# Kernel tuning notes

Hardware: AMD Instinct MI355X
Metric: run time of the kernel (lower is better)

The kernel has to match this reference:

```python
import jax, jax.numpy as jnp
import numpy as np
import math

B, S, K, D, H, LH, W, L = 8, 2048, 128, 512, 8, 4, 128, 4
DH = D // H           # 64, head dim
NW = S // W           # 16 windows
NUM_STEPS = 1000
RESCALE = 4000.0


def setup_inputs() -> dict:
    key = jax.random.key(0)
    ks = iter(jax.random.split(key, 48))
    def rn(shape, s=0.02):
        return jax.random.normal(next(ks), shape, dtype=jnp.float32) * s
    return {
        "x": jax.random.normal(next(ks), (B, S, K), dtype=jnp.float32),
        "t": jax.random.randint(next(ks), (B,), 0, NUM_STEPS, dtype=jnp.int32),
        "token_w": rn((K, D)), "token_b": jnp.zeros((D,), jnp.float32),
        "ax1": rn((NW, D), 1.0), "ax2": rn((W, D), 1.0),
        "time_w1": rn((D, 4 * D)), "time_b1": jnp.zeros((4 * D,), jnp.float32),
        "time_w2": rn((4 * D, D)), "time_b2": jnp.zeros((D,), jnp.float32),
        "ln1_g": jnp.ones((L, D), jnp.float32), "ln1_b": jnp.zeros((L, D), jnp.float32),
        "wq": rn((L, D, D)), "wk": rn((L, D, D)), "wv": rn((L, D, D)),
        "wo": rn((L, D, D)), "wo_b": jnp.zeros((L, D), jnp.float32),
        "ln2_g": jnp.ones((L, D), jnp.float32), "ln2_b": jnp.zeros((L, D), jnp.float32),
        "ff_w1": rn((L, D, 4 * D)), "ff_b1": jnp.zeros((L, 4 * D), jnp.float32),
        "ff_w2": rn((L, 4 * D, D)), "ff_b2": jnp.zeros((L, D), jnp.float32),
        "norm_g": jnp.ones((D,), jnp.float32), "norm_b": jnp.zeros((D,), jnp.float32),
        "out_w": rn((D, K)), "out_b": jnp.zeros((K,), jnp.float32),
        "alpha": jax.random.normal(next(ks), (1,), dtype=jnp.float32),
    }


def _layernorm(x, g, b, eps=1e-5):
    mu = x.mean(-1, keepdims=True)
    var = ((x - mu) ** 2).mean(-1, keepdims=True)
    return (x - mu) * jax.lax.rsqrt(var + eps) * g + b


def _mish(x):
    return x * jnp.tanh(jax.nn.softplus(x))


def _sinusoidal(t):
    # SinusoidalPosEmb(dim=D, num_steps=NUM_STEPS, rescale_steps=4000)
    tt = t.astype(jnp.float32) / NUM_STEPS * RESCALE
    half = D // 2
    freqs = jnp.exp(jnp.arange(half, dtype=jnp.float32) * (-math.log(10000.0) / (half - 1)))
    e = tt[:, None] * freqs[None, :]
    return jnp.concatenate([jnp.sin(e), jnp.cos(e)], axis=-1)  # (B, D)


def _linear_attn(q, k, v):
    # non-causal kernelized linear attention; q,k,v: (B, h, S, dh)
    scale = DH ** -0.25
    q = jax.nn.softmax(q * scale, axis=-1)   # softmax over feature dim
    k = jax.nn.softmax(k * scale, axis=-2)   # softmax over sequence dim
    ctx = jnp.einsum('bhnd,bhne->bhde', k, v)
    return jnp.einsum('bhnd,bhde->bhne', q, ctx)


def _local_attn(q, k, v):
    # windowed softmax attention, window W, look_backward=1, look_forward=1
    b, h = q.shape[0], q.shape[1]
    qw = q.reshape(b, h, NW, W, DH) * (DH ** -0.5)
    def look_around(x):
        xw = x.reshape(b, h, NW, W, DH)
        xp = jnp.pad(xw, ((0, 0), (0, 0), (1, 1), (0, 0), (0, 0)))
        # keys of windows [i-1, i, i+1] -> (b, h, NW, 3W, dh)
        return jnp.concatenate([xp[:, :, :-2], xp[:, :, 1:-1], xp[:, :, 2:]], axis=3)
    kw, vw = look_around(k), look_around(v)
    win = jnp.arange(NW)[:, None] + (jnp.arange(3 * W) // W)[None, :] - 1  # (NW, 3W)
    valid = (win >= 0) & (win < NW)
    dots = jnp.einsum('bhnwd,bhnkd->bhnwk', qw, kw)
    mask_value = -jnp.finfo(dots.dtype).max
    dots = jnp.where(valid[None, None, :, None, :], dots, mask_value)
    attn = jax.nn.softmax(dots, axis=-1)
    out = jnp.einsum('bhnwk,bhnkd->bhnwd', attn, vw)
    return out.reshape(b, h, S, DH)


def reference(x, t, token_w, token_b, ax1, ax2, time_w1, time_b1, time_w2, time_b2,
              ln1_g, ln1_b, wq, wk, wv, wo, wo_b, ln2_g, ln2_b,
              ff_w1, ff_b1, ff_w2, ff_b2, norm_g, norm_b, out_w, out_b, alpha):
    te = _sinusoidal(t)
    te = _mish(te @ time_w1 + time_b1) @ time_w2 + time_b2          # (B, D)
    h = x @ token_w + token_b                                        # token embedding
    pos = (ax1[:, None, :] + ax2[None, :, :]).reshape(S, D)          # axial pos emb (summed)
    h = h + pos[None] + te[:, None, :]
    for l in range(L):
        n = _layernorm(h, ln1_g[l], ln1_b[l])
        def split_heads(y):
            return y.reshape(B, S, H, DH).transpose(0, 2, 1, 3)
        q = split_heads(n @ wq[l]); k = split_heads(n @ wk[l]); v = split_heads(n @ wv[l])
        lo = _local_attn(q[:, :LH], k[:, :LH], v[:, :LH])            # local heads first
        gl = _linear_attn(q[:, LH:], k[:, LH:], v[:, LH:])           # global linear-attn heads
        a = jnp.concatenate([lo, gl], axis=1).transpose(0, 2, 1, 3).reshape(B, S, D)
        h = h + a @ wo[l] + wo_b[l]
        n = _layernorm(h, ln2_g[l], ln2_b[l])
        h = h + jax.nn.gelu(n @ ff_w1[l] + ff_b1[l], approximate=False) @ ff_w2[l] + ff_b2[l]
    out = _layernorm(h, norm_g, norm_b) @ out_w + out_b              # (B, S, K)
    return alpha * out.transpose(0, 2, 1)                            # permute + Rezero -> (B, K, S)
```

## Files before the change

### kernel.cpp

```cpp
#include <hip/hip_runtime.h>

typedef __bf16 bf16;
typedef float f32x4 __attribute__((ext_vector_type(4)));
typedef __bf16 b8v __attribute__((ext_vector_type(8)));
typedef __bf16 b4v __attribute__((ext_vector_type(4)));

#define S_LEN 2048
#define DMODEL 512
#define KDIM 128
#define NWIN 16
#define WIN 128
#define QKVS 1536

__device__ inline f32x4 mfma16(b8v a, b8v b, f32x4 c) {
  return __builtin_amdgcn_mfma_f32_16x16x32_bf16(a, b, c, 0, 0, 0);
}

__device__ inline void gload16(const bf16* g, bf16* l) {
  __builtin_amdgcn_global_load_lds(
      (const __attribute__((address_space(1))) void*)g,
      (__attribute__((address_space(3))) void*)l, 16, 0, 0);
}

template<int N>
__device__ inline void waitvm() { asm volatile("s_waitcnt vmcnt(%0)" :: "n"(N) : "memory"); }
template<int N>
__device__ inline void waitlgkm() { asm volatile("s_waitcnt lgkmcnt(%0)" :: "n"(N) : "memory"); }
__device__ inline void barrier_raw() { asm volatile("s_barrier" ::: "memory"); }


__global__ __launch_bounds__(256) void conv_kernel(const float* __restrict__ in, bf16* __restrict__ out, int n) {
  int i4 = (blockIdx.x * 256 + threadIdx.x) * 4;
  if (i4 < n) {
    float4 v = *(const float4*)(in + i4);
    b4v o; o[0] = (bf16)v.x; o[1] = (bf16)v.y; o[2] = (bf16)v.z; o[3] = (bf16)v.w;
    *(b4v*)(out + i4) = o;
  }
}

__global__ __launch_bounds__(256) void convT_kernel(const float* __restrict__ W, bf16* __restrict__ WT,
                                                    int Kd, int N, size_t in_ls, size_t out_ls) {
  __shared__ float tile[32][33];
  int k0 = blockIdx.x * 32, n0 = blockIdx.y * 32;
  const float* Wl = W + (size_t)blockIdx.z * in_ls;
  bf16* WTl = WT + (size_t)blockIdx.z * out_ls;
  int tx = threadIdx.x & 31, ty = threadIdx.x >> 5;
  #pragma unroll
  for (int i = 0; i < 4; i++)
    tile[ty + i*8][tx] = Wl[(size_t)(k0 + ty + i*8) * N + n0 + tx];
  __syncthreads();
  #pragma unroll
  for (int i = 0; i < 4; i++)
    WTl[(size_t)(n0 + ty + i*8) * Kd + k0 + tx] = (bf16)tile[tx][ty + i*8];
}


__global__ __launch_bounds__(256) void time1_kernel(const int* __restrict__ t,
    const float* __restrict__ w1, const float* __restrict__ b1, float* __restrict__ te1) {
  __shared__ float te[512];
  __shared__ float red[4][64];
  int b = blockIdx.x >> 5;
  int c0 = (blockIdx.x & 31) * 64;
  int tid = threadIdx.x;
  float tt = (float)t[b] * 4.0f;
  {
    float fr = expf((float)tid * (-9.210340371976184f / 255.0f));
    float e = tt * fr;
    te[tid] = sinf(e);
    te[tid + 256] = cosf(e);
  }
  __syncthreads();
  int lane = tid & 63, wv = tid >> 6;
  float acc = 0.f;
  const float* wcol = w1 + (size_t)(wv * 128) * 2048 + c0 + lane;
  for (int dd = 0; dd < 128; dd++) acc = fmaf(te[wv * 128 + dd], wcol[(size_t)dd * 2048], acc);
  red[wv][lane] = acc;
  __syncthreads();
  if (tid < 64) {
    float a = red[0][tid] + red[1][tid] + red[2][tid] + red[3][tid] + b1[c0 + tid];
    float sp = (a > 20.f) ? a : log1pf(expf(a));
    te1[b * 2048 + c0 + tid] = a * tanhf(sp);
  }
}

__global__ __launch_bounds__(256) void time2_kernel(const float* __restrict__ te1,
    const float* __restrict__ w2, const float* __restrict__ b2, float* __restrict__ te2) {
  __shared__ float hb[2048];
  __shared__ float red[4][64];
  int b = blockIdx.x >> 3;
  int c0 = (blockIdx.x & 7) * 64;
  int tid = threadIdx.x;
  for (int i = tid; i < 2048; i += 256) hb[i] = te1[b * 2048 + i];
  __syncthreads();
  int lane = tid & 63, wv = tid >> 6;
  float acc = 0.f;
  const float* wcol = w2 + (size_t)(wv * 512) * 512 + c0 + lane;
  for (int dd = 0; dd < 512; dd++) acc = fmaf(hb[wv * 512 + dd], wcol[(size_t)dd * 512], acc);
  red[wv][lane] = acc;
  __syncthreads();
  if (tid < 64)
    te2[b * 512 + c0 + tid] = red[0][tid] + red[1][tid] + red[2][tid] + red[3][tid] + b2[c0 + tid];
}


__global__ __launch_bounds__(256) void ln_kernel(const float* __restrict__ hsrc,
    const float* __restrict__ gg, const float* __restrict__ bb, bf16* __restrict__ out) {
  int row = blockIdx.x * 4 + (threadIdx.x >> 6);
  int lane = threadIdx.x & 63;
  const float* hr = hsrc + (size_t)row * 512 + lane * 8;
  float4 v0 = *(const float4*)hr;
  float4 v1 = *(const float4*)(hr + 4);
  float xv[8] = {v0.x, v0.y, v0.z, v0.w, v1.x, v1.y, v1.z, v1.w};
  float s = 0.f;
  #pragma unroll
  for (int j = 0; j < 8; j++) s += xv[j];
  #pragma unroll
  for (int off = 1; off < 64; off <<= 1) s += __shfl_xor(s, off);
  float mu = s * (1.f / 512.f);
  float vs = 0.f;
  #pragma unroll
  for (int j = 0; j < 8; j++) { float dd = xv[j] - mu; vs += dd * dd; }
  #pragma unroll
  for (int off = 1; off < 64; off <<= 1) vs += __shfl_xor(vs, off);
  float rstd = 1.f / sqrtf(vs * (1.f / 512.f) + 1e-5f);
  int dbase = lane * 8;
  bf16* orow = out + (size_t)row * 512 + dbase;
  #pragma unroll
  for (int j = 0; j < 8; j++)
    orow[j] = (bf16)((xv[j] - mu) * rstd * gg[dbase + j] + bb[dbase + j]);
}

template<int EPI, int BM, int BN>
__global__ __launch_bounds__(512, 2) void gemm3_kernel(
    const bf16* __restrict__ A, const bf16* __restrict__ BT,
    const float* __restrict__ bias, float* __restrict__ Cf, bf16* __restrict__ Cb,
    int N, int Kd, int nbx) {
  constexpr int LA = BM / 128;
  constexpr int LB = BN / 128;
  constexpr int LPI = LA + LB;
  constexpr int EA = BM * 32;
  constexpr int EB = BN * 32;
  constexpr int ER = EA + EB;
  constexpr int MF = BM / 32;
  constexpr int NF = BN / 64;
  __shared__ bf16 lds[ER * 3];
  int tid = threadIdx.x;
  int lane = tid & 63, wid = tid >> 6;
  int g = lane >> 4, lr = lane & 15;
  int wm = wid >> 2, wn = wid & 3;
  int p = blockIdx.x;
  int cpx = (int)gridDim.x >> 3;
  int vid = (p & 7) * cpx + (p >> 3);
  int m0 = (vid / nbx) * BM;
  int n0 = (vid % nbx) * BN;
  f32x4 acc[MF][NF] = {};
  int rl = tid >> 2;
  int csw = ((tid & 3) ^ ((rl >> 1) & 3)) * 8;
  const bf16* pa = A + (size_t)(m0 + rl) * Kd + csw;
  const bf16* pb = BT + (size_t)(n0 + rl) * Kd + csw;
  int NT = Kd >> 5;
  auto stage = [&](int t, int buf) {
    int k0 = t << 5;
    bf16* base = lds + buf * ER + (wid << 9);
    #pragma unroll
    for (int rr = 0; rr < LA; rr++)
      gload16(pa + (size_t)(rr * 128) * Kd + k0, base + rr * 4096);
    #pragma unroll
    for (int rr = 0; rr < LB; rr++)
      gload16(pb + (size_t)(rr * 128) * Kd + k0, base + EA + rr * 4096);
  };
  stage(0, 0);
  stage(1, 1);
  for (int kt = 0; kt < NT; ++kt) {
    if (kt + 1 < NT) waitvm<LPI>();
    else             waitvm<0>();
    barrier_raw();
    const bf16* ba = lds + (kt % 3) * ER;
    const bf16* bb = ba + EA;
    if (kt + 2 < NT) stage(kt + 2, (kt + 2) % 3);
    b8v af[MF], bfr[NF];
    #pragma unroll
    for (int i = 0; i < MF; i++) {
      int ra = wm * (BM / 2) + i * 16 + lr;
      af[i] = *(const b8v*)(ba + ra * 32 + ((g * 8) ^ (((ra >> 1) & 3) << 3)));
    }
    #pragma unroll
    for (int j0 = 0; j0 < 2; j0++) {
      int rb = wn * (BN / 4) + j0 * 16 + lr;
      bfr[j0] = *(const b8v*)(bb + rb * 32 + ((g * 8) ^ (((rb >> 1) & 3) << 3)));
    }
    waitlgkm<0>();
    __builtin_amdgcn_sched_barrier(0);
    __builtin_amdgcn_s_setprio(1);
    #pragma unroll
    for (int i = 0; i < MF; i++) acc[i][0] = mfma16(af[i], bfr[0], acc[i][0]);
    __builtin_amdgcn_s_setprio(0);
    #pragma unroll
    for (int j = 1; j < NF; j++) {
      if (j + 1 < NF) {
        int rb = wn * (BN / 4) + (j + 1) * 16 + lr;
        bfr[j + 1] = *(const b8v*)(bb + rb * 32 + ((g * 8) ^ (((rb >> 1) & 3) << 3)));
        waitlgkm<1>();
      } else {
        waitlgkm<0>();
      }
      __builtin_amdgcn_sched_barrier(0);
      __builtin_amdgcn_s_setprio(1);
      #pragma unroll
      for (int i = 0; i < MF; i++) acc[i][j] = mfma16(af[i], bfr[j], acc[i][j]);
      __builtin_amdgcn_s_setprio(0);
    }
  }
  #pragma unroll
  for (int i = 0; i < MF; i++) {
    #pragma unroll
    for (int j = 0; j < NF; j++) {
      int col = n0 + wn * (BN / 4) + j * 16 + lr;
      float bv = (EPI != 0) ? bias[col] : 0.0f;
      #pragma unroll
      for (int r = 0; r < 4; r++) {
        int row = m0 + wm * (BM / 2) + i * 16 + g * 4 + r;
        float v = acc[i][j][r] + bv;
        if (EPI == 0) {
          Cb[(size_t)row * N + col] = (bf16)v;
        } else if (EPI == 2) {
          Cf[(size_t)row * N + col] += v;
        } else if (EPI == 3) {
          float u = 1.5957691216057308f * (v + 0.044715f * v * v * v);
          float ge = v / (1.0f + __expf(-u));
          Cb[(size_t)row * N + col] = (bf16)ge;
        }
      }
    }
  }
}

template<int EPI>
__global__ __launch_bounds__(256) void gemm_kernel(
    const bf16* __restrict__ A, const bf16* __restrict__ BT,
    const float* __restrict__ bias, float* __restrict__ Cf, bf16* __restrict__ Cb,
    int N, int Kd, int nbx,
    const float* __restrict__ q1, const float* __restrict__ q2, const float* __restrict__ q3,
    const float* __restrict__ alphap) {
  __shared__ bf16 As[2][4096];
  __shared__ bf16 Bs[2][4096];
  int tid = threadIdx.x;
  int lane = tid & 63, wid = tid >> 6;
  int g = lane >> 4, lr = lane & 15;
  int wm = wid >> 1, wn = wid & 1;
  int p = blockIdx.x;
  int cpx = (int)gridDim.x >> 3;
  int vid = (p & 7) * cpx + (p >> 3);
  int m0 = (vid / nbx) * 128;
  int n0 = (vid % nbx) * 128;
  f32x4 acc[4][4] = {};
  int srow = wid * 16 + (lane >> 2);
  int scol = (lane & 3) * 8;
  const bf16* pa = A + (size_t)(m0 + srow) * Kd + scol;
  const bf16* pb = BT + (size_t)(n0 + srow) * Kd + scol;
  const size_t rstep = (size_t)64 * Kd;
  int nt = Kd >> 5;
  auto stage = [&](int buf, int k0) {
    bf16* lA = &As[buf][wid * 512];
    bf16* lB = &Bs[buf][wid * 512];
    gload16(pa + k0, lA);
    gload16(pa + rstep + k0, lA + 2048);
    gload16(pb + k0, lB);
    gload16(pb + rstep + k0, lB + 2048);
  };
  stage(0, 0);
  __syncthreads();
  int cur = 0;
  for (int t = 0; t < nt; ++t) {
    if (t + 1 < nt) stage(cur ^ 1, (t + 1) * 32);
    b8v af[4], bfv[4];
    #pragma unroll
    for (int i = 0; i < 4; i++) af[i]  = *(const b8v*)&As[cur][(wm * 64 + i * 16 + lr) * 32 + g * 8];
    #pragma unroll
    for (int i = 0; i < 4; i++) bfv[i] = *(const b8v*)&Bs[cur][(wn * 64 + i * 16 + lr) * 32 + g * 8];
    #pragma unroll
    for (int mf = 0; mf < 4; mf++)
      #pragma unroll
      for (int nf = 0; nf < 4; nf++)
        acc[mf][nf] = mfma16(af[mf], bfv[nf], acc[mf][nf]);
    __syncthreads();
    cur ^= 1;
  }
  if constexpr (EPI == 4) {
    __shared__ float Ts[32][130];
    float alp = alphap[0];
    int b_ = m0 >> 11, sb = m0 & 2047;
    #pragma unroll
    for (int cg = 0; cg < 4; cg++) {
      __syncthreads();
      if (wn == (cg >> 1)) {
        #pragma unroll
        for (int nfi = 0; nfi < 2; nfi++) {
          int nf = (cg & 1) * 2 + nfi;
          int cl = nfi * 16 + lr;
          float bv = bias[cg * 32 + cl];
          #pragma unroll
          for (int mf = 0; mf < 4; mf++)
            #pragma unroll
            for (int r = 0; r < 4; r++)
              Ts[cl][wm * 64 + mf * 16 + g * 4 + r] = alp * (acc[mf][nf][r] + bv);
        }
      }
      __syncthreads();
      int cl = tid >> 3, soff = (tid & 7) * 16;
      int col = cg * 32 + cl;
      float* dst = Cf + (size_t)b_ * (KDIM * S_LEN) + (size_t)col * S_LEN + sb + soff;
      #pragma unroll
      for (int q4 = 0; q4 < 4; q4++) {
        float4 v = {Ts[cl][soff + q4*4], Ts[cl][soff + q4*4 + 1], Ts[cl][soff + q4*4 + 2], Ts[cl][soff + q4*4 + 3]};
        *(float4*)(dst + q4 * 4) = v;
      }
    }
    return;
  }
  #pragma unroll
  for (int mf = 0; mf < 4; mf++) {
    #pragma unroll
    for (int nf = 0; nf < 4; nf++) {
      int col = n0 + wn * 64 + nf * 16 + lr;
      float bv = bias[col];
      #pragma unroll
      for (int r = 0; r < 4; r++) {
        int row = m0 + wm * 64 + mf * 16 + g * 4 + r;
        float v = acc[mf][nf][r] + bv;
        if (EPI == 5) {
          int b_ = row >> 11, s_ = row & 2047;
          float pv = q1[(s_ >> 7) * 512 + col] + q2[(s_ & 127) * 512 + col] + q3[b_ * 512 + col];
          Cf[(size_t)row * N + col] = v + pv;
        }
      }
    }
  }
}

__global__ __launch_bounds__(256) void locattn_kernel(
    const bf16* __restrict__ qkv, bf16* __restrict__ ab) {
  __shared__ bf16 Ks[128][72];
  __shared__ bf16 Vt[64][136];
  __shared__ bf16 Ps[4][32][136];
  int w = blockIdx.x;
  int b = blockIdx.y >> 2, hh = blockIdx.y & 3;
  int tid = threadIdx.x, wid = tid >> 6, lane = tid & 63;
  int g = lane >> 4, lr = lane & 15;
  const size_t rowb = (size_t)b * S_LEN * QKVS;
  int qrow0 = w * WIN + wid * 32;
  b8v qf[2][2];
  #pragma unroll
  for (int mf = 0; mf < 2; mf++)
    #pragma unroll
    for (int kf = 0; kf < 2; kf++)
      qf[mf][kf] = *(const b8v*)(qkv + rowb + (size_t)(qrow0 + mf * 16 + lr) * QKVS + hh * 64 + kf * 32 + g * 8);
  float mrun[2][4], lrun[2][4];
  f32x4 oacc[2][4] = {};
  #pragma unroll
  for (int mf = 0; mf < 2; mf++)
    #pragma unroll
    for (int r = 0; r < 4; r++) { mrun[mf][r] = -3e38f; lrun[mf][r] = 0.f; }
  for (int c = 0; c < 3; c++) {
    int wc = w - 1 + c;
    if (wc < 0 || wc >= NWIN) continue;
    __syncthreads();
    {
      int row = tid >> 1, f0 = (tid & 1) * 32;
      const bf16* kp = qkv + rowb + (size_t)(wc * WIN + row) * QKVS + 512 + hh * 64 + f0;
      #pragma unroll
      for (int i = 0; i < 4; i++)
        *(b8v*)&Ks[row][f0 + i * 8] = *(const b8v*)(kp + i * 8);
      const bf16* vp = qkv + rowb + (size_t)(wc * WIN + row) * QKVS + 1024 + hh * 64 + f0;
      #pragma unroll
      for (int i = 0; i < 4; i++) {
        b8v vv = *(const b8v*)(vp + i * 8);
        #pragma unroll
        for (int j = 0; j < 8; j++) Vt[f0 + i * 8 + j][row] = vv[j];
      }
    }
    __syncthreads();
    f32x4 sc[2][8] = {};
    #pragma unroll
    for (int nf = 0; nf < 8; nf++) {
      #pragma unroll
      for (int kf = 0; kf < 2; kf++) {
        b8v kfr = *(const b8v*)&Ks[nf * 16 + lr][kf * 32 + g * 8];
        sc[0][nf] = mfma16(qf[0][kf], kfr, sc[0][nf]);
        sc[1][nf] = mfma16(qf[1][kf], kfr, sc[1][nf]);
      }
    }
    #pragma unroll
    for (int mf = 0; mf < 2; mf++) {
      #pragma unroll
      for (int r = 0; r < 4; r++) {
        float cm = -3e38f;
        #pragma unroll
        for (int nf = 0; nf < 8; nf++) { sc[mf][nf][r] *= 0.125f; cm = fmaxf(cm, sc[mf][nf][r]); }
        cm = fmaxf(cm, __shfl_xor(cm, 1));
        cm = fmaxf(cm, __shfl_xor(cm, 2));
        cm = fmaxf(cm, __shfl_xor(cm, 4));
        cm = fmaxf(cm, __shfl_xor(cm, 8));
        float mnew = fmaxf(mrun[mf][r], cm);
        float corr = __expf(mrun[mf][r] - mnew);
        float rs = 0.f;
        #pragma unroll
        for (int nf = 0; nf < 8; nf++) { float p = __expf(sc[mf][nf][r] - mnew); sc[mf][nf][r] = p; rs += p; }
        rs += __shfl_xor(rs, 1); rs += __shfl_xor(rs, 2);
        rs += __shfl_xor(rs, 4); rs += __shfl_xor(rs, 8);
        lrun[mf][r] = lrun[mf][r] * corr + rs;
        mrun[mf][r] = mnew;
        #pragma unroll
        for (int vf = 0; vf < 4; vf++) oacc[mf][vf][r] *= corr;
      }
    }
    #pragma unroll
    for (int mf = 0; mf < 2; mf++)
      #pragma unroll
      for (int nf = 0; nf < 8; nf++)
        #pragma unroll
        for (int r = 0; r < 4; r++)
          Ps[wid][mf * 16 + g * 4 + r][nf * 16 + lr] = (bf16)sc[mf][nf][r];
    #pragma unroll
    for (int kf2 = 0; kf2 < 4; kf2++) {
      b8v pa0 = *(const b8v*)&Ps[wid][lr][kf2 * 32 + g * 8];
      b8v pa1 = *(const b8v*)&Ps[wid][16 + lr][kf2 * 32 + g * 8];
      #pragma unroll
      for (int vf = 0; vf < 4; vf++) {
        b8v vv = *(const b8v*)&Vt[vf * 16 + lr][kf2 * 32 + g * 8];
        oacc[0][vf] = mfma16(pa0, vv, oacc[0][vf]);
        oacc[1][vf] = mfma16(pa1, vv, oacc[1][vf]);
      }
    }
  }
  #pragma unroll
  for (int mf = 0; mf < 2; mf++) {
    #pragma unroll
    for (int r = 0; r < 4; r++) {
      float inv = 1.0f / lrun[mf][r];
      int row = qrow0 + mf * 16 + g * 4 + r;
      #pragma unroll
      for (int vf = 0; vf < 4; vf++)
        ab[(size_t)b * S_LEN * DMODEL + (size_t)row * DMODEL + hh * 64 + vf * 16 + lr] = (bf16)(oacc[mf][vf][r] * inv);
    }
  }
}


__global__ __launch_bounds__(256) void la2_kernel(const bf16* __restrict__ qkv,
    float* __restrict__ part, float* __restrict__ psum) {
  int ch = blockIdx.x, bh = blockIdx.y;
  int b = bh >> 2, hh = bh & 3;
  __shared__ float ke[128][65];
  __shared__ float vsh[128][65];
  __shared__ float red[4][64];
  int tid = threadIdx.x;
  const float scale = 0.35355339059327373f;
  const size_t base = ((size_t)b * S_LEN + (size_t)ch * 128) * QKVS;
  const bf16* kp = qkv + base + 768 + hh * 64;
  const bf16* vp = qkv + base + 1280 + hh * 64;
  for (int i = tid; i < 1024; i += 256) {
    int s = i >> 3, d0 = (i & 7) * 8;
    b8v kv = *(const b8v*)(kp + (size_t)s * QKVS + d0);
    b8v vv = *(const b8v*)(vp + (size_t)s * QKVS + d0);
    #pragma unroll
    for (int j = 0; j < 8; j++) {
      ke[s][d0 + j] = __expf((float)kv[j] * scale);
      vsh[s][d0 + j] = (float)vv[j];
    }
  }
  __syncthreads();
  int d = tid & 63, sg = tid >> 6;
  float ps = 0.f;
  for (int s = sg * 32; s < sg * 32 + 32; s++) ps += ke[s][d];
  red[sg][d] = ps;
  int e = tid & 63, dg = tid >> 6;
  float accv[16] = {};
  for (int s = 0; s < 128; s++) {
    float vv2 = vsh[s][e];
    #pragma unroll
    for (int i = 0; i < 16; i++) accv[i] = fmaf(ke[s][dg * 16 + i], vv2, accv[i]);
  }
  __syncthreads();
  float* pp = part + ((size_t)ch * 32 + bh) * 4096 + (size_t)dg * 16 * 64 + e;
  #pragma unroll
  for (int i = 0; i < 16; i++) pp[i * 64] = accv[i];
  if (tid < 64)
    psum[((size_t)ch * 32 + bh) * 64 + tid] = red[0][tid] + red[1][tid] + red[2][tid] + red[3][tid];
}

__global__ __launch_bounds__(256) void la2b_kernel(const float* __restrict__ part,
    const float* __restrict__ psum, float* __restrict__ ctx) {
  int idx = blockIdx.x * 256 + threadIdx.x;
  int bh = idx >> 12;
  int d = (idx >> 6) & 63;
  float s = 0.f, cs = 0.f;
  for (int c = 0; c < 16; c++) {
    s += part[(size_t)c * 131072 + idx];
    cs += psum[(size_t)(c * 32 + bh) * 64 + d];
  }
  ctx[idx] = s / cs;
}

__global__ __launch_bounds__(256) void la3_kernel(const bf16* __restrict__ qkv,
    const float* __restrict__ ctx, bf16* __restrict__ ab) {
  int ch = blockIdx.x, bh = blockIdx.y;
  int b = bh >> 2, hh = bh & 3;
  __shared__ float cs[64][65];
  int tid = threadIdx.x;
  for (int i = tid; i < 4096; i += 256) cs[i >> 6][i & 63] = ctx[(size_t)bh * 4096 + i];
  __syncthreads();
  int s = ch * 128 + (tid >> 1);
  int e0 = (tid & 1) * 32;
  const float scale = 0.35355339059327373f;
  const bf16* qr = qkv + ((size_t)b * S_LEN + s) * QKVS + 256 + hh * 64;
  float qv[64];
  float mx = -3e38f;
  #pragma unroll
  for (int i = 0; i < 8; i++) {
    b8v qq = *(const b8v*)(qr + i * 8);
    #pragma unroll
    for (int j = 0; j < 8; j++) { qv[i * 8 + j] = (float)qq[j] * scale; mx = fmaxf(mx, qv[i * 8 + j]); }
  }
  float sum = 0.f;
  #pragma unroll
  for (int dd = 0; dd < 64; dd++) { qv[dd] = __expf(qv[dd] - mx); sum += qv[dd]; }
  float inv = 1.f / sum;
  float o[32] = {};
  #pragma unroll
  for (int dd = 0; dd < 64; dd++) {
    float qq = qv[dd] * inv;
    #pragma unroll
    for (int j = 0; j < 32; j++) o[j] = fmaf(qq, cs[dd][e0 + j], o[j]);
  }
  bf16* op = ab + ((size_t)b * S_LEN + s) * DMODEL + 256 + hh * 64 + e0;
  #pragma unroll
  for (int j = 0; j < 32; j++) op[j] = (bf16)o[j];
}


extern "C" void kernel_launch(void* const* d_in, const int* in_sizes, int n_in,
                              void* d_out, int out_size, void* d_ws, size_t ws_size,
                              hipStream_t stream) {
  (void)in_sizes; (void)n_in; (void)out_size; (void)ws_size;
  const float* x_f     = (const float*)d_in[0];
  const int*   t_i     = (const int*)  d_in[1];
  const float* token_w = (const float*)d_in[2];
  const float* token_b = (const float*)d_in[3];
  const float* ax1     = (const float*)d_in[4];
  const float* ax2     = (const float*)d_in[5];
  const float* time_w1 = (const float*)d_in[6];
  const float* time_b1 = (const float*)d_in[7];
  const float* time_w2 = (const float*)d_in[8];
  const float* time_b2 = (const float*)d_in[9];
  const float* ln1_g   = (const float*)d_in[10];
  const float* ln1_b   = (const float*)d_in[11];
  const float* wq      = (const float*)d_in[12];
  const float* wk      = (const float*)d_in[13];
  const float* wv      = (const float*)d_in[14];
  const float* wo      = (const float*)d_in[15];
  const float* wo_b    = (const float*)d_in[16];
  const float* ln2_g   = (const float*)d_in[17];
  const float* ln2_b   = (const float*)d_in[18];
  const float* ff_w1   = (const float*)d_in[19];
  const float* ff_b1   = (const float*)d_in[20];
  const float* ff_w2   = (const float*)d_in[21];
  const float* ff_b2   = (const float*)d_in[22];
  const float* norm_g  = (const float*)d_in[23];
  const float* norm_b  = (const float*)d_in[24];
  const float* out_w   = (const float*)d_in[25];
  const float* out_b   = (const float*)d_in[26];
  const float* alpha   = (const float*)d_in[27];

  char* ws = (char*)d_ws;
  float* h      = (float*)(ws + 0);
  float* te1    = (float*)(ws + 33554432);
  float* te2    = (float*)(ws + 33619968);
  float* psum   = (float*)(ws + 33636352);
  float* ctx    = (float*)(ws + 33767424);
  float* part   = (float*)(ws + 34291712);
  bf16* nbuf    = (bf16*)(ws + 42680320);
  bf16* qkvb    = (bf16*)(ws + 59457536);
  bf16* abuf    = (bf16*)(ws + 109789184);
  bf16* gbuf    = qkvb;
  bf16* xw      = (bf16*)(ws + 126566400);
  bf16* token_wT= (bf16*)(ws + 130760704);
  bf16* wqkvT   = (bf16*)(ws + 130891776);
  bf16* woT     = (bf16*)(ws + 137183232);
  bf16* ff1T    = (bf16*)(ws + 139280384);
  bf16* ff2T    = (bf16*)(ws + 147668992);
  bf16* outwT   = (bf16*)(ws + 156057600);

  conv_kernel<<<2048, 256, 0, stream>>>(x_f, xw, 2097152);
  convT_kernel<<<dim3(4, 16, 1),  256, 0, stream>>>(token_w, token_wT, 128, 512, 65536, 65536);
  convT_kernel<<<dim3(16, 16, 4), 256, 0, stream>>>(wq, wqkvT,           512, 512, 262144, 786432);
  convT_kernel<<<dim3(16, 16, 4), 256, 0, stream>>>(wk, wqkvT + 262144,  512, 512, 262144, 786432);
  convT_kernel<<<dim3(16, 16, 4), 256, 0, stream>>>(wv, wqkvT + 524288,  512, 512, 262144, 786432);
  convT_kernel<<<dim3(16, 16, 4), 256, 0, stream>>>(wo, woT, 512, 512, 262144, 262144);
  convT_kernel<<<dim3(16, 64, 4), 256, 0, stream>>>(ff_w1, ff1T, 512, 2048, 1048576, 1048576);
  convT_kernel<<<dim3(64, 16, 4), 256, 0, stream>>>(ff_w2, ff2T, 2048, 512, 1048576, 1048576);
  convT_kernel<<<dim3(16, 4, 1),  256, 0, stream>>>(out_w, outwT, 512, 128, 65536, 65536);

  time1_kernel<<<256, 256, 0, stream>>>(t_i, time_w1, time_b1, te1);
  time2_kernel<<<64, 256, 0, stream>>>(te1, time_w2, time_b2, te2);

  gemm_kernel<5><<<512, 256, 0, stream>>>(xw, token_wT, token_b, h, nullptr, 512, 128, 4, ax1, ax2, te2, nullptr);

  for (int l = 0; l < 4; l++) {
    ln_kernel<<<4096, 256, 0, stream>>>(h, ln1_g + l * 512, ln1_b + l * 512, nbuf);
    gemm3_kernel<0, 128, 256><<<768, 512, 0, stream>>>(nbuf, wqkvT + (size_t)l * 786432, nullptr, nullptr, qkvb, 1536, 512, 6);
    locattn_kernel<<<dim3(16, 32), 256, 0, stream>>>(qkvb, abuf);
    la2_kernel<<<dim3(16, 32), 256, 0, stream>>>(qkvb, part, psum);
    la2b_kernel<<<512, 256, 0, stream>>>(part, psum, ctx);
    la3_kernel<<<dim3(16, 32), 256, 0, stream>>>(qkvb, ctx, abuf);
    gemm3_kernel<2, 128, 256><<<256, 512, 0, stream>>>(abuf, woT + (size_t)l * 262144, wo_b + l * 512, h, nullptr, 512, 512, 2);
    ln_kernel<<<4096, 256, 0, stream>>>(h, ln2_g + l * 512, ln2_b + l * 512, nbuf);
    gemm3_kernel<3, 256, 256><<<512, 512, 0, stream>>>(nbuf, ff1T + (size_t)l * 1048576, ff_b1 + l * 2048, nullptr, gbuf, 2048, 512, 8);
    gemm3_kernel<2, 128, 256><<<256, 512, 0, stream>>>(gbuf, ff2T + (size_t)l * 1048576, ff_b2 + l * 512, h, nullptr, 512, 2048, 2);
  }

  ln_kernel<<<4096, 256, 0, stream>>>(h, norm_g, norm_b, nbuf);
  gemm_kernel<4><<<128, 256, 0, stream>>>(nbuf, outwT, out_b, (float*)d_out, nullptr, 128, 512, 1, nullptr, nullptr, nullptr, alpha);
}
```

Baseline: 1.092 ms.

## Store residual stream in bf16 and merge QKV/O weight transposes

The fp32 residual buffer h becomes bf16. This halves the traffic for the layernorm reads and for the read-modify-write residual adds in the O-projection and FF2 GEMM epilogues, and the workspace offsets are recomputed to match. The separate transpose launches for wq/wk/wv/wo are also merged into one convT4 launch. The cost is accuracy: residual accumulation in bf16 over 4 layers loses precision and may exceed the tolerance.

```diff
diff --git a/kernel.cpp b/kernel.cpp
--- a/kernel.cpp
+++ b/kernel.cpp
@@ -52,6 +52,27 @@
   #pragma unroll
   for (int i = 0; i < 4; i++)
     WTl[(size_t)(n0 + ty + i*8) * Kd + k0 + tx] = (bf16)tile[tx][ty + i*8];
+}
+
+__global__ __launch_bounds__(256) void convT4_kernel(
+    const float* __restrict__ wq, const float* __restrict__ wk,
+    const float* __restrict__ wv, const float* __restrict__ wo,
+    bf16* __restrict__ wqkvT, bf16* __restrict__ woT) {
+  __shared__ float tile[32][33];
+  int z = blockIdx.z, layer = z >> 2, which = z & 3;
+  const float* W = (which == 0 ? wq : which == 1 ? wk : which == 2 ? wv : wo)
+                   + (size_t)layer * 262144;
+  bf16* WT = (which < 3) ? (wqkvT + (size_t)layer * 786432 + (size_t)which * 262144)
+                         : (woT + (size_t)layer * 262144);
+  int k0 = blockIdx.x * 32, n0 = blockIdx.y * 32;
+  int tx = threadIdx.x & 31, ty = threadIdx.x >> 5;
+  #pragma unroll
+  for (int i = 0; i < 4; i++)
+    tile[ty + i*8][tx] = W[(size_t)(k0 + ty + i*8) * 512 + n0 + tx];
+  __syncthreads();
+  #pragma unroll
+  for (int i = 0; i < 4; i++)
+    WT[(size_t)(n0 + ty + i*8) * 512 + k0 + tx] = (bf16)tile[tx][ty + i*8];
 }
 
 
@@ -103,14 +124,15 @@
 }
 
 
-__global__ __launch_bounds__(256) void ln_kernel(const float* __restrict__ hsrc,
+__global__ __launch_bounds__(256) void ln_kernel(const bf16* __restrict__ hsrc,
     const float* __restrict__ gg, const float* __restrict__ bb, bf16* __restrict__ out) {
   int row = blockIdx.x * 4 + (threadIdx.x >> 6);
   int lane = threadIdx.x & 63;
-  const float* hr = hsrc + (size_t)row * 512 + lane * 8;
-  float4 v0 = *(const float4*)hr;
-  float4 v1 = *(const float4*)(hr + 4);
-  float xv[8] = {v0.x, v0.y, v0.z, v0.w, v1.x, v1.y, v1.z, v1.w};
+  const bf16* hr = hsrc + (size_t)row * 512 + lane * 8;
+  b8v hv = *(const b8v*)hr;
+  float xv[8];
+  #pragma unroll
+  for (int j = 0; j < 8; j++) xv[j] = (float)hv[j];
   float s = 0.f;
   #pragma unroll
   for (int j = 0; j < 8; j++) s += xv[j];
@@ -133,7 +155,7 @@
 template<int EPI, int BM, int BN>
 __global__ __launch_bounds__(512, 2) void gemm3_kernel(
     const bf16* __restrict__ A, const bf16* __restrict__ BT,
-    const float* __restrict__ bias, float* __restrict__ Cf, bf16* __restrict__ Cb,
+    const float* __restrict__ bias, bf16* __restrict__ Cb,
     int N, int Kd, int nbx) {
   constexpr int LA = BM / 128;
   constexpr int LB = BN / 128;
@@ -224,7 +246,8 @@
         if (EPI == 0) {
           Cb[(size_t)row * N + col] = (bf16)v;
         } else if (EPI == 2) {
-          Cf[(size_t)row * N + col] += v;
+          size_t idx = (size_t)row * N + col;
+          Cb[idx] = (bf16)((float)Cb[idx] + v);
         } else if (EPI == 3) {
           float u = 1.5957691216057308f * (v + 0.044715f * v * v * v);
           float ge = v / (1.0f + __expf(-u));
@@ -331,7 +354,7 @@
         if (EPI == 5) {
           int b_ = row >> 11, s_ = row & 2047;
           float pv = q1[(s_ >> 7) * 512 + col] + q2[(s_ & 127) * 512 + col] + q3[b_ * 512 + col];
-          Cf[(size_t)row * N + col] = v + pv;
+          Cb[(size_t)row * N + col] = (bf16)(v + pv);
         }
       }
     }
@@ -573,30 +596,27 @@
   const float* alpha   = (const float*)d_in[27];
 
   char* ws = (char*)d_ws;
-  float* h      = (float*)(ws + 0);
-  float* te1    = (float*)(ws + 33554432);
-  float* te2    = (float*)(ws + 33619968);
-  float* psum   = (float*)(ws + 33636352);
-  float* ctx    = (float*)(ws + 33767424);
-  float* part   = (float*)(ws + 34291712);
-  bf16* nbuf    = (bf16*)(ws + 42680320);
-  bf16* qkvb    = (bf16*)(ws + 59457536);
-  bf16* abuf    = (bf16*)(ws + 109789184);
+  bf16*  h      = (bf16*)(ws + 0);
+  float* te1    = (float*)(ws + 16777216);
+  float* te2    = (float*)(ws + 16842752);
+  float* psum   = (float*)(ws + 16859136);
+  float* ctx    = (float*)(ws + 16990208);
+  float* part   = (float*)(ws + 17514496);
+  bf16* nbuf    = (bf16*)(ws + 25903104);
+  bf16* qkvb    = (bf16*)(ws + 42680320);
+  bf16* abuf    = (bf16*)(ws + 93011968);
   bf16* gbuf    = qkvb;
-  bf16* xw      = (bf16*)(ws + 126566400);
-  bf16* token_wT= (bf16*)(ws + 130760704);
-  bf16* wqkvT   = (bf16*)(ws + 130891776);
-  bf16* woT     = (bf16*)(ws + 137183232);
-  bf16* ff1T    = (bf16*)(ws + 139280384);
-  bf16* ff2T    = (bf16*)(ws + 147668992);
-  bf16* outwT   = (bf16*)(ws + 156057600);
+  bf16* xw      = (bf16*)(ws + 109789184);
+  bf16* token_wT= (bf16*)(ws + 113983488);
+  bf16* wqkvT   = (bf16*)(ws + 114114560);
+  bf16* woT     = (bf16*)(ws + 120406016);
+  bf16* ff1T    = (bf16*)(ws + 122503168);
+  bf16* ff2T    = (bf16*)(ws + 130891776);
+  bf16* outwT   = (bf16*)(ws + 139280384);
 
   conv_kernel<<<2048, 256, 0, stream>>>(x_f, xw, 2097152);
   convT_kernel<<<dim3(4, 16, 1),  256, 0, stream>>>(token_w, token_wT, 128, 512, 65536, 65536);
-  convT_kernel<<<dim3(16, 16, 4), 256, 0, stream>>>(wq, wqkvT,           512, 512, 262144, 786432);
-  convT_kernel<<<dim3(16, 16, 4), 256, 0, stream>>>(wk, wqkvT + 262144,  512, 512, 262144, 786432);
-  convT_kernel<<<dim3(16, 16, 4), 256, 0, stream>>>(wv, wqkvT + 524288,  512, 512, 262144, 786432);
-  convT_kernel<<<dim3(16, 16, 4), 256, 0, stream>>>(wo, woT, 512, 512, 262144, 262144);
+  convT4_kernel<<<dim3(16, 16, 16), 256, 0, stream>>>(wq, wk, wv, wo, wqkvT, woT);
   convT_kernel<<<dim3(16, 64, 4), 256, 0, stream>>>(ff_w1, ff1T, 512, 2048, 1048576, 1048576);
   convT_kernel<<<dim3(64, 16, 4), 256, 0, stream>>>(ff_w2, ff2T, 2048, 512, 1048576, 1048576);
   convT_kernel<<<dim3(16, 4, 1),  256, 0, stream>>>(out_w, outwT, 512, 128, 65536, 65536);
@@ -604,19 +624,19 @@
   time1_kernel<<<256, 256, 0, stream>>>(t_i, time_w1, time_b1, te1);
   time2_kernel<<<64, 256, 0, stream>>>(te1, time_w2, time_b2, te2);
 
-  gemm_kernel<5><<<512, 256, 0, stream>>>(xw, token_wT, token_b, h, nullptr, 512, 128, 4, ax1, ax2, te2, nullptr);
+  gemm_kernel<5><<<512, 256, 0, stream>>>(xw, token_wT, token_b, nullptr, h, 512, 128, 4, ax1, ax2, te2, nullptr);
 
   for (int l = 0; l < 4; l++) {
     ln_kernel<<<4096, 256, 0, stream>>>(h, ln1_g + l * 512, ln1_b + l * 512, nbuf);
-    gemm3_kernel<0, 128, 256><<<768, 512, 0, stream>>>(nbuf, wqkvT + (size_t)l * 786432, nullptr, nullptr, qkvb, 1536, 512, 6);
+    gemm3_kernel<0, 128, 256><<<768, 512, 0, stream>>>(nbuf, wqkvT + (size_t)l * 786432, nullptr, qkvb, 1536, 512, 6);
     locattn_kernel<<<dim3(16, 32), 256, 0, stream>>>(qkvb, abuf);
     la2_kernel<<<dim3(16, 32), 256, 0, stream>>>(qkvb, part, psum);
     la2b_kernel<<<512, 256, 0, stream>>>(part, psum, ctx);
     la3_kernel<<<dim3(16, 32), 256, 0, stream>>>(qkvb, ctx, abuf);
-    gemm3_kernel<2, 128, 256><<<256, 512, 0, stream>>>(abuf, woT + (size_t)l * 262144, wo_b + l * 512, h, nullptr, 512, 512, 2);
+    gemm3_kernel<2, 128, 256><<<256, 512, 0, stream>>>(abuf, woT + (size_t)l * 262144, wo_b + l * 512, h, 512, 512, 2);
     ln_kernel<<<4096, 256, 0, stream>>>(h, ln2_g + l * 512, ln2_b + l * 512, nbuf);
-    gemm3_kernel<3, 256, 256><<<512, 512, 0, stream>>>(nbuf, ff1T + (size_t)l * 1048576, ff_b1 + l * 2048, nullptr, gbuf, 2048, 512, 8);
-    gemm3_kernel<2, 128, 256><<<256, 512, 0, stream>>>(gbuf, ff2T + (size_t)l * 1048576, ff_b2 + l * 512, h, nullptr, 512, 2048, 2);
+    gemm3_kernel<3, 256, 256><<<512, 512, 0, stream>>>(nbuf, ff1T + (size_t)l * 1048576, ff_b1 + l * 2048, gbuf, 2048, 512, 8);
+    gemm3_kernel<2, 128, 256><<<256, 512, 0, stream>>>(gbuf, ff2T + (size_t)l * 1048576, ff_b2 + l * 512, h, 512, 2048, 2);
   }
 
   ln_kernel<<<4096, 256, 0, stream>>>(h, norm_g, norm_b, nbuf);
```

New measurement: 1.039 ms. 4.8% less time.
